# Kernel tuning notes

Hardware: AMD Instinct MI355X
Metric: run time of the kernel (lower is better)

The kernel has to match this reference:

```python
import jax, jax.numpy as jnp
import numpy as np

SURROGATE_BETA = 10.0

@jax.custom_jvp
def spike_fn(x):
    return jnp.heaviside(x, 1.0)

@spike_fn.defjvp
def _spike_fn_jvp(primals, tangents):
    (x,) = primals
    (x_dot,) = tangents
    return spike_fn(x), x_dot / (1.0 + SURROGATE_BETA * jnp.abs(x))


def setup_inputs() -> dict:
    key = jax.random.key(0)
    k1, k2 = jax.random.split(key)
    B, T, H = 64, 1000, 512
    x = jax.random.normal(k1, (B, T, H), dtype=jnp.float32)
    # learnable decay constants (alpha, beta), will be clamped to [0.5, 1.0]
    decay_constants = jnp.array([0.95, 0.9], dtype=jnp.float32)
    threshold = jnp.array(1.0, dtype=jnp.float32)
    return {"x": x, "decay_constants": decay_constants, "threshold": threshold}


def reference(x, decay_constants, threshold):
    # x: (B, T, H). LIF recurrence over time, vectorized over (B, H).
    alpha = jax.lax.clamp(0.5, decay_constants[0], 1.0)  # membrane decay
    beta = jax.lax.clamp(0.5, decay_constants[1], 1.0)   # synaptic decay
    B, T, H = x.shape
    x_tbh = jnp.swapaxes(x, 0, 1)  # (T, B, H) for scan over time

    def step(carry, x_t):
        mem_pot, syn_curr, spike_out = carry
        # reset_val is None -> reset_pot = mem_pot * spike_out
        reset_pot = jax.lax.stop_gradient(mem_pot * spike_out)  # stop_reset_grad=True
        mem_pot = mem_pot - reset_pot
        mem_pot = alpha * mem_pot + (1.0 - alpha) * syn_curr
        syn_curr = beta * syn_curr + (1.0 - beta) * x_t
        spike_out = spike_fn(mem_pot - threshold)
        return (mem_pot, syn_curr, spike_out), spike_out

    zeros = jnp.zeros((B, H), dtype=jnp.float32)
    init = (zeros, zeros, zeros)
    _, spikes = jax.lax.scan(step, init, x_tbh)  # spikes: (T, B, H)
    return jnp.swapaxes(spikes, 0, 1)  # (B, T, H)
```

## Files before the change

kernel.cpp:

```cpp
#include <hip/hip_runtime.h>


#define LIF_B 64
#define LIF_T 1000
#define LIF_H 512
#define LIF_U 8

__global__ __launch_bounds__(64) void lif_kernel(
    const float* __restrict__ x,
    const float* __restrict__ decay,
    const float* __restrict__ thr_p,
    float* __restrict__ out)
{
    const int n = blockIdx.x * blockDim.x + threadIdx.x;
    const int b = n >> 9;
    const int h = n & (LIF_H - 1);

    const float alpha = fminf(fmaxf(decay[0], 0.5f), 1.0f);
    const float beta  = fminf(fmaxf(decay[1], 0.5f), 1.0f);
    const float oma = __fsub_rn(1.0f, alpha);
    const float omb = __fsub_rn(1.0f, beta);
    const float thr = thr_p[0];

    const size_t base = (size_t)b * LIF_T * LIF_H + h;
    const float* xp = x + base;
    float* op = out + base;

    float mem = 0.0f, syn = 0.0f, spike = 0.0f;

    float b0[LIF_U], b1[LIF_U], b2[LIF_U];
    #pragma unroll
    for (int u = 0; u < LIF_U; ++u) b0[u] = xp[(size_t)u * LIF_H];
    #pragma unroll
    for (int u = 0; u < LIF_U; ++u) b1[u] = xp[(size_t)(LIF_U + u) * LIF_H];

    for (int t = 0; t < LIF_T; t += LIF_U) {
        const int tp = t + 2 * LIF_U;
        if (tp < LIF_T) {
            #pragma unroll
            for (int u = 0; u < LIF_U; ++u)
                b2[u] = xp[(size_t)(tp + u) * LIF_H];
        }
        #pragma unroll
        for (int u = 0; u < LIF_U; ++u) {
            const float xv = b0[u];
            const float reset = __fmul_rn(mem, spike);
            mem = __fsub_rn(mem, reset);
            mem = __fadd_rn(__fmul_rn(alpha, mem), __fmul_rn(oma, syn));
            syn = __fadd_rn(__fmul_rn(beta, syn), __fmul_rn(omb, xv));
            spike = (__fsub_rn(mem, thr) >= 0.0f) ? 1.0f : 0.0f;
            op[(size_t)(t + u) * LIF_H] = spike;
        }
        #pragma unroll
        for (int u = 0; u < LIF_U; ++u) { b0[u] = b1[u]; b1[u] = b2[u]; }
    }
}

extern "C" void kernel_launch(void* const* d_in, const int* in_sizes, int n_in,
                              void* d_out, int out_size, void* d_ws, size_t ws_size,
                              hipStream_t stream) {
    const float* x     = (const float*)d_in[0];
    const float* decay = (const float*)d_in[1];
    const float* thr   = (const float*)d_in[2];
    float* out = (float*)d_out;

    const int total = LIF_B * LIF_H;
    const int block = 64;
    const int grid  = total / block;
    lif_kernel<<<grid, block, 0, stream>>>(x, decay, thr, out);
}
```

Measured before the change: 291.7 us.

## Stream inputs via async global-to-LDS loads with 4-deep buffered pipeline

Replaces per-thread register prefetch of x with asynchronous global_load_lds transfers into a 4-stage LDS ring buffer, 40 timesteps per stage, using explicit vmcnt waits to overlap loads with the sequential recurrence. Loads become 16-byte wide per lane covering 4 rows per instruction. Outputs use nontemporal stores. It relies on hand-written waitcnt counts and inline asm LDS reads, which are fragile and tied to exact instruction counts.

```diff
diff --git a/kernel.cpp b/kernel.cpp
--- a/kernel.cpp
+++ b/kernel.cpp
@@ -1,20 +1,26 @@
 #include <hip/hip_runtime.h>
 
 
-#define LIF_B 64
 #define LIF_T 1000
 #define LIF_H 512
-#define LIF_U 8
+#define U 40
+#define NB 4
 
-__global__ __launch_bounds__(64) void lif_kernel(
+#define AS1 __attribute__((address_space(1)))
+#define AS3 __attribute__((address_space(3)))
+
+__global__ __launch_bounds__(64, 1) void lif_kernel(
     const float* __restrict__ x,
     const float* __restrict__ decay,
     const float* __restrict__ thr_p,
     float* __restrict__ out)
 {
-    const int n = blockIdx.x * blockDim.x + threadIdx.x;
-    const int b = n >> 9;
-    const int h = n & (LIF_H - 1);
+    __shared__ float lds[NB][U][64];
+
+    const int lane = threadIdx.x;
+    const int blk  = blockIdx.x;
+    const int b    = blk >> 3;
+    const int h0   = (blk & 7) << 6;
 
     const float alpha = fminf(fmaxf(decay[0], 0.5f), 1.0f);
     const float beta  = fminf(fmaxf(decay[1], 0.5f), 1.0f);
@@ -22,38 +28,66 @@
     const float omb = __fsub_rn(1.0f, beta);
     const float thr = thr_p[0];
 
-    const size_t base = (size_t)b * LIF_T * LIF_H + h;
-    const float* xp = x + base;
-    float* op = out + base;
+    const float* gsrc = x + ((size_t)b * LIF_T + (lane >> 4)) * LIF_H
+                          + h0 + (lane & 15) * 4;
+    float* op = out + (size_t)b * LIF_T * LIF_H + h0 + lane;
 
-    float mem = 0.0f, syn = 0.0f, spike = 0.0f;
+    const unsigned lbase = (unsigned)(size_t)(const AS3 void*)&lds[0][0][0]
+                         + (unsigned)lane * 4u;
 
-    float b0[LIF_U], b1[LIF_U], b2[LIF_U];
-    #pragma unroll
-    for (int u = 0; u < LIF_U; ++u) b0[u] = xp[(size_t)u * LIF_H];
-    #pragma unroll
-    for (int u = 0; u < LIF_U; ++u) b1[u] = xp[(size_t)(LIF_U + u) * LIF_H];
+    float mem = 0.f, syn = 0.f, spike = 0.f;
 
-    for (int t = 0; t < LIF_T; t += LIF_U) {
-        const int tp = t + 2 * LIF_U;
-        if (tp < LIF_T) {
-            #pragma unroll
-            for (int u = 0; u < LIF_U; ++u)
-                b2[u] = xp[(size_t)(tp + u) * LIF_H];
-        }
-        #pragma unroll
-        for (int u = 0; u < LIF_U; ++u) {
-            const float xv = b0[u];
-            const float reset = __fmul_rn(mem, spike);
-            mem = __fsub_rn(mem, reset);
-            mem = __fadd_rn(__fmul_rn(alpha, mem), __fmul_rn(oma, syn));
-            syn = __fadd_rn(__fmul_rn(beta, syn), __fmul_rn(omb, xv));
-            spike = (__fsub_rn(mem, thr) >= 0.0f) ? 1.0f : 0.0f;
-            op[(size_t)(t + u) * LIF_H] = spike;
-        }
-        #pragma unroll
-        for (int u = 0; u < LIF_U; ++u) { b0[u] = b1[u]; b1[u] = b2[u]; }
+#define ISSUE(c, buf) do {                                                  \
+    _Pragma("unroll")                                                       \
+    for (int g = 0; g < U / 4; ++g)                                         \
+        __builtin_amdgcn_global_load_lds(                                   \
+            (AS1 void*)(gsrc + (size_t)((c) * U + g * 4) * LIF_H),          \
+            (AS3 void*)&lds[buf][g * 4][0], 16, 0, 0);                      \
+} while (0)
+
+#define VWAIT(nn) do {                                                      \
+    asm volatile("s_waitcnt vmcnt(" #nn ")" ::: "memory");                  \
+    __builtin_amdgcn_sched_barrier(0); } while (0)
+
+#define COMPUTE(c, buf) do {                                                \
+    float xv[U];                                                            \
+    _Pragma("unroll")                                                       \
+    for (int u = 0; u < U; ++u)                                             \
+        asm volatile("ds_read_b32 %0, %1" : "=v"(xv[u])                     \
+            : "v"(lbase + (unsigned)(((buf) * U + u) * 256)));              \
+    asm volatile("s_waitcnt lgkmcnt(0)" ::: "memory");                      \
+    __builtin_amdgcn_sched_barrier(0);                                      \
+    _Pragma("unroll")                                                       \
+    for (int u = 0; u < U; ++u) {                                           \
+        const float r_ = __fmul_rn(mem, spike);                             \
+        mem = __fsub_rn(mem, r_);                                           \
+        mem = __fadd_rn(__fmul_rn(alpha, mem), __fmul_rn(oma, syn));        \
+        syn = __fadd_rn(__fmul_rn(beta, syn), __fmul_rn(omb, xv[u]));       \
+        spike = (__fsub_rn(mem, thr) >= 0.0f) ? 1.0f : 0.0f;                \
+        __builtin_nontemporal_store(spike,                                  \
+            op + (size_t)((c) * U + u) * LIF_H);                            \
+    }                                                                       \
+} while (0)
+
+    ISSUE(0, 0); ISSUE(1, 1); ISSUE(2, 2); ISSUE(3, 3);
+
+    #pragma unroll 1
+    for (int c = 0; c <= 16; c += 4) {
+        VWAIT(30); COMPUTE(c + 0, 0); ISSUE(c + 4, 0);
+        VWAIT(30); COMPUTE(c + 1, 1); ISSUE(c + 5, 1);
+        VWAIT(30); COMPUTE(c + 2, 2); ISSUE(c + 6, 2);
+        VWAIT(30); COMPUTE(c + 3, 3); ISSUE(c + 7, 3);
     }
+
+    VWAIT(30); COMPUTE(20, 0); ISSUE(24, 0);
+    VWAIT(30); COMPUTE(21, 1);
+    VWAIT(20); COMPUTE(22, 2);
+    VWAIT(10); COMPUTE(23, 3);
+    VWAIT(0);  COMPUTE(24, 0);
+
+#undef ISSUE
+#undef VWAIT
+#undef COMPUTE
 }
 
 extern "C" void kernel_launch(void* const* d_in, const int* in_sizes, int n_in,
@@ -64,8 +98,6 @@
     const float* thr   = (const float*)d_in[2];
     float* out = (float*)d_out;
 
-    const int total = LIF_B * LIF_H;
-    const int block = 64;
-    const int grid  = total / block;
-    lif_kernel<<<grid, block, 0, stream>>>(x, decay, thr, out);
+    const int grid = 512;
+    lif_kernel<<<grid, 64, 0, stream>>>(x, decay, thr, out);
 }
```

New measurement: 236.9 us. 1.23x faster.
